# Kernel optimization log

Measured on AMD Instinct MI355X. Metric: run time of the kernel, lower is better.

The kernel has to match this reference:

```python
import jax, jax.numpy as jnp
import numpy as np

NUM_FIELDS = 40
EMBED_DIM = 64
IN_SUB = 40
OUT_SUB = 40
BATCH = 256


def setup_inputs() -> dict:
    key = jax.random.key(0)
    k0, k1 = jax.random.split(key)
    B0 = jax.random.normal(k0, (BATCH, NUM_FIELDS, EMBED_DIM), dtype=jnp.float32)
    Bi = jax.random.normal(k1, (BATCH, IN_SUB, EMBED_DIM), dtype=jnp.float32)
    # parameters, initialized exactly as in the torch module
    W = jnp.tile(jnp.eye(EMBED_DIM, dtype=jnp.float32)[None], (OUT_SUB, 1, 1))  # (n, D, D)
    alpha = jnp.ones((NUM_FIELDS, IN_SUB, OUT_SUB), dtype=jnp.float32)          # (f, i, n)
    h = jnp.ones((OUT_SUB, EMBED_DIM, 1), dtype=jnp.float32)                    # (n, D, 1)
    return {"B0": B0, "Bi": Bi, "W": W, "alpha": alpha, "h": h}


def reference(B0, Bi, W, alpha, h):
    # Math of the original: fusion[b,n,D,d] = sum_{f,i} B0[b,f,D]*Bi[b,i,d]*alpha[f,i,n]
    # (equivalent to the 5D outer product contracted with alpha, but never
    #  materializes the (b,f,i,D,D) tensor).
    fusion = jnp.einsum('bfD,bid,fin->bnDd', B0, Bi, alpha)  # (b, n, D, D)
    # elementwise scale by W then project with h: out[b,n,D] = sum_d fusion*W*h
    out = jnp.einsum('bnDd,nDd,nd->bnD', fusion, W, h[..., 0])
    return out
```

## Files before the change

### kernel.cpp

```cpp
#include <hip/hip_runtime.h>
#include <hip/hip_bf16.h>

#define NF 40
#define NI 40
#define NN 40
#define ED 64
#define NB 256

typedef __attribute__((ext_vector_type(8))) short   short8;
typedef __attribute__((ext_vector_type(8))) __bf16  bf16x8;
typedef __attribute__((ext_vector_type(4))) float   f32x4;

__device__ __forceinline__ unsigned short f2bf(float x) {
    union { float f; unsigned u; } v; v.f = x;
    unsigned r = v.u + 0x7FFFu + ((v.u >> 16) & 1u);
    return (unsigned short)(r >> 16);
}

__device__ __forceinline__ bf16x8 ld_frag(const unsigned short* p) {
    return __builtin_bit_cast(bf16x8, *(const short8*)p);
}

__device__ __forceinline__ f32x4 mfma16(bf16x8 a, bf16x8 b, f32x4 c) {
    return __builtin_amdgcn_mfma_f32_16x16x32_bf16(a, b, c, 0, 0, 0);
}

#define WHP_N (64 * 64)
#define ALP_N (48 * 64)

__global__ __launch_bounds__(256) void gif_prep4(
        const float* __restrict__ W, const float* __restrict__ alpha,
        const float* __restrict__ h,
        unsigned short* __restrict__ whp, unsigned short* __restrict__ alp) {
    const int x = blockIdx.x;
    const int t = threadIdx.x;
    if (x < NN) {
        const int n = x;
        for (int idx = t; idx < 64 * 64; idx += 256) {
            int d = idx & 63;
            whp[n * WHP_N + idx] = f2bf(W[n * ED * ED + idx] * h[n * ED + d]);
        }
        for (int idx = t; idx < 8 * 64; idx += 256)
            alp[n * ALP_N + (40 + (idx >> 6)) * 64 + (idx & 63)] = 0;
        for (int idx = t; idx < 40 * 24; idx += 256) {
            int i = idx / 24, f = 40 + idx - i * 24;
            alp[n * ALP_N + i * 64 + f] = 0;
        }
    } else {
        const int f = x - NN;
        for (int idx = t; idx < NI * NN; idx += 256) {
            int i = idx / NN, n = idx - i * NN;
            alp[n * ALP_N + i * 64 + f] = f2bf(alpha[(f * NI + i) * NN + n]);
        }
    }
}

#define PSM 72
__global__ __launch_bounds__(256, 3) void gif_main6(
        const float* __restrict__ B0, const float* __restrict__ Bi,
        const unsigned short* __restrict__ whp,
        const unsigned short* __restrict__ alp,
        float* __restrict__ out) {
    const int bg = blockIdx.x;
    const int ng = blockIdx.y;
    const int t = threadIdx.x;
    const int lane = t & 63, w = t >> 6;
    const int quad = lane >> 4, l15 = lane & 15, fo = quad * 8;
    const int n = ng * 4 + w;

    __shared__ __align__(16) unsigned short sBi[48 * PSM];
    __shared__ __align__(16) unsigned short sBT[64 * PSM];

    bf16x8 alA[3][2], whB[4][2];
    {
        const unsigned short* ap = alp + n * ALP_N;
        const unsigned short* wp = whp + n * WHP_N;
#pragma unroll
        for (int m = 0; m < 3; ++m)
#pragma unroll
            for (int s = 0; s < 2; ++s)
                alA[m][s] = ld_frag(&ap[(m * 16 + l15) * 64 + s * 32 + fo]);
#pragma unroll
        for (int tt = 0; tt < 4; ++tt)
#pragma unroll
            for (int s = 0; s < 2; ++s)
                whB[tt][s] = ld_frag(&wp[(tt * 16 + l15) * 64 + s * 32 + fo]);
    }

    for (int j = 0; j < 4; ++j) {
        const int b = bg * 4 + j;
        if (j) __syncthreads();

        const float* bi = Bi + (size_t)b * NI * ED;
        const float* b0 = B0 + (size_t)b * NF * ED;
        for (int idx = t; idx < NI * ED; idx += 256) {
            int i = idx >> 6, d = idx & 63;
            sBi[i * PSM + d] = f2bf(bi[idx]);
        }
        for (int idx = t; idx < 8 * 64; idx += 256)
            sBi[(40 + (idx >> 6)) * PSM + (idx & 63)] = 0;
        for (int idx = t; idx < NF * ED; idx += 256) {
            int f = idx >> 6, D = idx & 63;
            sBT[D * PSM + f] = f2bf(b0[idx]);
        }
        for (int idx = t; idx < 64 * 24; idx += 256) {
            int D = idx / 24, f = 40 + idx - D * 24;
            sBT[D * PSM + f] = 0;
        }
        __syncthreads();

        bf16x8 biA[3][2];
#pragma unroll
        for (int m = 0; m < 3; ++m)
#pragma unroll
            for (int s = 0; s < 2; ++s)
                biA[m][s] = ld_frag(&sBi[(m * 16 + l15) * PSM + s * 32 + fo]);

        float p[4];
#pragma unroll
        for (int tt = 0; tt < 4; ++tt) {
            bf16x8 bb0 = ld_frag(&sBT[(tt * 16 + l15) * PSM + fo]);
            bf16x8 bb1 = ld_frag(&sBT[(tt * 16 + l15) * PSM + 32 + fo]);
            float acc = 0.f;
#pragma unroll
            for (int m = 0; m < 3; ++m) {
                f32x4 z = {0.f, 0.f, 0.f, 0.f};
                f32x4 T = mfma16(biA[m][0], whB[tt][0], z);
                T = mfma16(biA[m][1], whB[tt][1], T);
                f32x4 G = mfma16(alA[m][0], bb0, z);
                G = mfma16(alA[m][1], bb1, G);
                acc += T[0] * G[0] + T[1] * G[1] + T[2] * G[2] + T[3] * G[3];
            }
            p[tt] = acc;
        }
#pragma unroll
        for (int tt = 0; tt < 4; ++tt) {
            p[tt] += __shfl_xor(p[tt], 16, 64);
            p[tt] += __shfl_xor(p[tt], 32, 64);
        }
        float v = (quad == 0) ? p[0] : (quad == 1) ? p[1] : (quad == 2) ? p[2] : p[3];
        out[((size_t)b * NN + n) * ED + lane] = v;
    }
}

#define PS 72
#define WH_N (ED * PS)
#define AL_N (48 * PS)

__global__ __launch_bounds__(256) void gif_prep(
        const float* __restrict__ W, const float* __restrict__ alpha,
        const float* __restrict__ h,
        unsigned short* __restrict__ whp, unsigned short* __restrict__ alp) {
    const int n = blockIdx.x;
    const int t0 = blockIdx.y * 256 + threadIdx.x;
    for (int idx = t0; idx < ED * PS; idx += 1024) {
        int D = idx / PS, c = idx - D * PS;
        float v = (c < ED) ? W[n * ED * ED + D * ED + c] * h[n * ED + c] : 0.f;
        whp[n * WH_N + idx] = f2bf(v);
    }
    for (int idx = t0; idx < 48 * PS; idx += 1024) {
        int i = idx / PS, c = idx - i * PS;
        float v = (i < NI && c < NF) ? alpha[(c * NI + i) * NN + n] : 0.f;
        alp[n * AL_N + idx] = f2bf(v);
    }
}

__device__ __forceinline__ bf16x8 mk_al_frag(const float* __restrict__ alpha,
        int n, int m, int s, int l15, int quad) {
    bf16x8 r;
    const int row = m * 16 + l15;
    const int f0 = s * 32 + quad * 8;
#pragma unroll
    for (int j = 0; j < 8; ++j) {
        const int f = f0 + j;
        float v = (row < NI && f < NF) ? alpha[(f * NI + row) * NN + n] : 0.f;
        r[j] = (__bf16)v;
    }
    return r;
}
__device__ __forceinline__ bf16x8 mk_wh_frag(const float* __restrict__ W,
        const float* __restrict__ h, int n, int tt, int s, int l15, int quad) {
    bf16x8 r;
    const int row = tt * 16 + l15;
    const int k0 = s * 32 + quad * 8;
#pragma unroll
    for (int j = 0; j < 8; ++j) {
        float v = W[n * ED * ED + row * ED + k0 + j] * h[n * ED + k0 + j];
        r[j] = (__bf16)v;
    }
    return r;
}

__global__ __launch_bounds__(256) void gif_mfma(
        const float* __restrict__ B0, const float* __restrict__ Bi,
        const unsigned short* __restrict__ whp, const unsigned short* __restrict__ alp,
        const float* __restrict__ W, const float* __restrict__ alpha,
        const float* __restrict__ h, int useWs, float* __restrict__ out) {
    const int q = blockIdx.x >> 8;
    const int b = blockIdx.x & 255;

    __shared__ __align__(16) unsigned short sBi[48 * PS];
    __shared__ __align__(16) unsigned short sBT[ED * PS];

    const int t = threadIdx.x;
    for (int idx = t; idx < 48 * PS; idx += 256) {
        int i = idx / PS, c = idx - i * PS;
        sBi[idx] = (i < NI && c < ED) ? f2bf(Bi[b * NI * ED + i * ED + c])
                                      : (unsigned short)0;
    }
    for (int idx = t; idx < ED * PS; idx += 256) {
        int D = idx / PS, c = idx - D * PS;
        sBT[idx] = (c < NF) ? f2bf(B0[b * NF * ED + c * ED + D])
                            : (unsigned short)0;
    }
    __syncthreads();

    const int lane = t & 63, w = t >> 6;
    const int quad = lane >> 4, l15 = lane & 15;
    const int fragoff = quad * 8;

    bf16x8 biA[3][2], b0B[4][2];
#pragma unroll
    for (int m = 0; m < 3; ++m)
#pragma unroll
        for (int s = 0; s < 2; ++s)
            biA[m][s] = ld_frag(&sBi[(m * 16 + l15) * PS + s * 32 + fragoff]);
#pragma unroll
    for (int tt = 0; tt < 4; ++tt)
#pragma unroll
        for (int s = 0; s < 2; ++s)
            b0B[tt][s] = ld_frag(&sBT[(tt * 16 + l15) * PS + s * 32 + fragoff]);

#pragma unroll
    for (int rep = 0; rep < 2; ++rep) {
        const int n = q * 8 + w + rep * 4;

        bf16x8 alA[3][2];
        if (useWs) {
#pragma unroll
            for (int m = 0; m < 3; ++m)
#pragma unroll
                for (int s = 0; s < 2; ++s)
                    alA[m][s] = ld_frag(&alp[n * AL_N + (m * 16 + l15) * PS + s * 32 + fragoff]);
        } else {
#pragma unroll
            for (int m = 0; m < 3; ++m)
#pragma unroll
                for (int s = 0; s < 2; ++s)
                    alA[m][s] = mk_al_frag(alpha, n, m, s, l15, quad);
        }

        float p[4];
#pragma unroll
        for (int tt = 0; tt < 4; ++tt) {
            bf16x8 whB2[2];
            if (useWs) {
                const unsigned short* wpp = &whp[n * WH_N + (tt * 16 + l15) * PS + fragoff];
                whB2[0] = ld_frag(wpp);
                whB2[1] = ld_frag(wpp + 32);
            } else {
                whB2[0] = mk_wh_frag(W, h, n, tt, 0, l15, quad);
                whB2[1] = mk_wh_frag(W, h, n, tt, 1, l15, quad);
            }
            float acc = 0.f;
#pragma unroll
            for (int m = 0; m < 3; ++m) {
                f32x4 z = {0.f, 0.f, 0.f, 0.f};
                f32x4 T = mfma16(biA[m][0], whB2[0], z);
                T = mfma16(biA[m][1], whB2[1], T);
                f32x4 G = mfma16(alA[m][0], b0B[tt][0], z);
                G = mfma16(alA[m][1], b0B[tt][1], G);
                acc += T[0] * G[0] + T[1] * G[1] + T[2] * G[2] + T[3] * G[3];
            }
            p[tt] = acc;
        }
#pragma unroll
        for (int tt = 0; tt < 4; ++tt) {
            p[tt] += __shfl_xor(p[tt], 16, 64);
            p[tt] += __shfl_xor(p[tt], 32, 64);
        }
        float v = (quad == 0) ? p[0] : (quad == 1) ? p[1] : (quad == 2) ? p[2] : p[3];
        out[(b * NN + n) * ED + lane] = v;
    }
}

extern "C" void kernel_launch(void* const* d_in, const int* in_sizes, int n_in,
                              void* d_out, int out_size, void* d_ws, size_t ws_size,
                              hipStream_t stream) {
    const float* B0    = (const float*)d_in[0];
    const float* Bi    = (const float*)d_in[1];
    const float* W     = (const float*)d_in[2];
    const float* alpha = (const float*)d_in[3];
    const float* h     = (const float*)d_in[4];
    float* out = (float*)d_out;

    const size_t need2 = (size_t)(NN * WHP_N + NN * ALP_N) * sizeof(unsigned short);
    if (ws_size >= need2) {
        unsigned short* whp = (unsigned short*)d_ws;
        unsigned short* alp = whp + (size_t)NN * WHP_N;
        gif_prep4<<<NN + NF, 256, 0, stream>>>(W, alpha, h, whp, alp);
        gif_main6<<<dim3(NB / 4, NN / 4), 256, 0, stream>>>(B0, Bi, whp, alp, out);
        return;
    }

    const size_t need1 = (size_t)(NN * WH_N + NN * AL_N) * sizeof(unsigned short);
    const int useWs = (ws_size >= need1) ? 1 : 0;
    unsigned short* whp = (unsigned short*)d_ws;
    unsigned short* alp = whp + (size_t)NN * WH_N;
    if (useWs) {
        gif_prep<<<dim3(NN, 4), 256, 0, stream>>>(W, alpha, h, whp, alp);
    }
    gif_mfma<<<5 * NB, 256, 0, stream>>>(B0, Bi, whp, alp, W, alpha, h, useWs, out);
}
```

Measured before the change: 97.76 us.

## Prefetch next batch tile into registers with float4 loads during MFMA compute

The main kernel now loads the next batch element's B0 and Bi rows into registers with float4 loads while the current element's MFMA work runs, then converts and writes them to shared memory between two barriers. Padding zeros are written once instead of every iteration, and the launch-bounds occupancy hint drops from 3 to 2 blocks to leave room for the prefetch registers. This is meant to hide global-load latency behind compute and to vectorize the loads. The cost is extra register pressure, lower occupancy and one additional barrier per iteration.

```diff
diff --git a/kernel.cpp b/kernel.cpp
--- a/kernel.cpp
+++ b/kernel.cpp
@@ -56,7 +56,7 @@
 }
 
 #define PSM 72
-__global__ __launch_bounds__(256, 3) void gif_main6(
+__global__ __launch_bounds__(256, 2) void gif_main8(
         const float* __restrict__ B0, const float* __restrict__ Bi,
         const unsigned short* __restrict__ whp,
         const unsigned short* __restrict__ alp,
@@ -71,6 +71,17 @@
     __shared__ __align__(16) unsigned short sBi[48 * PSM];
     __shared__ __align__(16) unsigned short sBT[64 * PSM];
 
+    float4 rbi[3], rb0[3];
+    {
+        const float4* biv = (const float4*)(Bi + (size_t)(bg * 4) * NI * ED);
+        const float4* b0v = (const float4*)(B0 + (size_t)(bg * 4) * NF * ED);
+#pragma unroll
+        for (int k = 0; k < 3; ++k) {
+            const int c = t + k * 256;
+            if (c < 640) { rbi[k] = biv[c]; rb0[k] = b0v[c]; }
+        }
+    }
+
     bf16x8 alA[3][2], whB[4][2];
     {
         const unsigned short* ap = alp + n * ALP_N;
@@ -87,27 +98,43 @@
                 whB[tt][s] = ld_frag(&wp[(tt * 16 + l15) * 64 + s * 32 + fo]);
     }
 
+    for (int idx = t; idx < 8 * 64; idx += 256)
+        sBi[(40 + (idx >> 6)) * PSM + (idx & 63)] = 0;
+    for (int idx = t; idx < 64 * 24; idx += 256) {
+        int D = idx / 24, f = 40 + idx - D * 24;
+        sBT[D * PSM + f] = 0;
+    }
+
+#pragma unroll
+    for (int k = 0; k < 3; ++k) {
+        const int c = t + k * 256;
+        if (c < 640) {
+            const int r = c >> 4, col = (c & 15) * 4;
+            ushort4 pk;
+            pk.x = f2bf(rbi[k].x); pk.y = f2bf(rbi[k].y);
+            pk.z = f2bf(rbi[k].z); pk.w = f2bf(rbi[k].w);
+            *(ushort4*)&sBi[r * PSM + col] = pk;
+            sBT[(col + 0) * PSM + r] = f2bf(rb0[k].x);
+            sBT[(col + 1) * PSM + r] = f2bf(rb0[k].y);
+            sBT[(col + 2) * PSM + r] = f2bf(rb0[k].z);
+            sBT[(col + 3) * PSM + r] = f2bf(rb0[k].w);
+        }
+    }
+    __syncthreads();
+
+#pragma unroll
     for (int j = 0; j < 4; ++j) {
         const int b = bg * 4 + j;
-        if (j) __syncthreads();
-
-        const float* bi = Bi + (size_t)b * NI * ED;
-        const float* b0 = B0 + (size_t)b * NF * ED;
-        for (int idx = t; idx < NI * ED; idx += 256) {
-            int i = idx >> 6, d = idx & 63;
-            sBi[i * PSM + d] = f2bf(bi[idx]);
-        }
-        for (int idx = t; idx < 8 * 64; idx += 256)
-            sBi[(40 + (idx >> 6)) * PSM + (idx & 63)] = 0;
-        for (int idx = t; idx < NF * ED; idx += 256) {
-            int f = idx >> 6, D = idx & 63;
-            sBT[D * PSM + f] = f2bf(b0[idx]);
-        }
-        for (int idx = t; idx < 64 * 24; idx += 256) {
-            int D = idx / 24, f = 40 + idx - D * 24;
-            sBT[D * PSM + f] = 0;
-        }
-        __syncthreads();
+
+        if (j < 3) {
+            const float4* biv = (const float4*)(Bi + (size_t)(b + 1) * NI * ED);
+            const float4* b0v = (const float4*)(B0 + (size_t)(b + 1) * NF * ED);
+#pragma unroll
+            for (int k = 0; k < 3; ++k) {
+                const int c = t + k * 256;
+                if (c < 640) { rbi[k] = biv[c]; rb0[k] = b0v[c]; }
+            }
+        }
 
         bf16x8 biA[3][2];
 #pragma unroll
@@ -140,6 +167,26 @@
         }
         float v = (quad == 0) ? p[0] : (quad == 1) ? p[1] : (quad == 2) ? p[2] : p[3];
         out[((size_t)b * NN + n) * ED + lane] = v;
+
+        if (j < 3) {
+            __syncthreads();
+#pragma unroll
+            for (int k = 0; k < 3; ++k) {
+                const int c = t + k * 256;
+                if (c < 640) {
+                    const int r = c >> 4, col = (c & 15) * 4;
+                    ushort4 pk;
+                    pk.x = f2bf(rbi[k].x); pk.y = f2bf(rbi[k].y);
+                    pk.z = f2bf(rbi[k].z); pk.w = f2bf(rbi[k].w);
+                    *(ushort4*)&sBi[r * PSM + col] = pk;
+                    sBT[(col + 0) * PSM + r] = f2bf(rb0[k].x);
+                    sBT[(col + 1) * PSM + r] = f2bf(rb0[k].y);
+                    sBT[(col + 2) * PSM + r] = f2bf(rb0[k].z);
+                    sBT[(col + 3) * PSM + r] = f2bf(rb0[k].w);
+                }
+            }
+            __syncthreads();
+        }
     }
 }
 
@@ -299,7 +346,7 @@
         unsigned short* whp = (unsigned short*)d_ws;
         unsigned short* alp = whp + (size_t)NN * WHP_N;
         gif_prep4<<<NN + NF, 256, 0, stream>>>(W, alpha, h, whp, alp);
-        gif_main6<<<dim3(NB / 4, NN / 4), 256, 0, stream>>>(B0, Bi, whp, alp, out);
+        gif_main8<<<dim3(64, 10), 256, 0, stream>>>(B0, Bi, whp, alp, out);
         return;
     }
 
```

Result: faster. 81.53 us (-16.6%).
